# Performance work log

Hardware: AMD Instinct MI355X
Metric: run time of the kernel (lower is better)

The kernel has to match this reference:

```python
import jax, jax.numpy as jnp
import numpy as np

B, T, V, E, H, L = 128, 512, 32000, 1024, 1024, 2

def setup_inputs() -> dict:
    key = jax.random.key(0)
    ks = jax.random.split(key, 6)
    g = lambda k, shape: (jax.random.normal(k, shape, jnp.float32) * 0.02)
    return {
        "X": jax.random.randint(ks[0], (B, T), 0, V, dtype=jnp.int32),
        "emb": g(ks[1], (V, E)),
        "Wx0": g(ks[2], (E, 3 * H)),
        "Wh0": g(ks[3], (H, 3 * H)),
        "b0": jnp.zeros((2, 3 * H), jnp.float32),
        "Wx1": g(ks[4], (H, 3 * H)),
        "Wh1": g(ks[5], (H, 3 * H)),
        "b1": jnp.zeros((2, 3 * H), jnp.float32),
    }

def _gru_cell(x, h, Wx, Wh, b):
    # Keras GRUCell, reset_after=True, gate order (z, r, n)
    gx = x @ Wx + b[0]          # [B, 3H]
    gh = h @ Wh + b[1]          # [B, 3H]
    xz, xr, xn = jnp.split(gx, 3, axis=-1)
    hz, hr, hn = jnp.split(gh, 3, axis=-1)
    z = jax.nn.sigmoid(xz + hz)
    r = jax.nn.sigmoid(xr + hr)
    n = jnp.tanh(xn + r * hn)
    return z * h + (1.0 - z) * n

def reference(X, emb, Wx0, Wh0, b0, Wx1, Wh1, b1):
    Xe = emb[X]                         # [B, T, E] embedding lookup
    params = ((Wx0, Wh0, b0), (Wx1, Wh1, b1))
    h_init = tuple(jnp.zeros((X.shape[0], H), Xe.dtype) for _ in range(L))

    def step(carry, x_t):
        new_hs = []
        inp = x_t
        for h_prev, (Wx, Wh, b) in zip(carry, params):
            h_new = _gru_cell(inp, h_prev, Wx, Wh, b)
            new_hs.append(h_new)
            inp = h_new
        return tuple(new_hs), inp       # top-layer output per step

    final_state, outs = jax.lax.scan(step, h_init, jnp.swapaxes(Xe, 0, 1))
    output = jnp.swapaxes(outs, 0, 1)   # [B, T, H], return_sequences=True
    return (output,) + final_state      # (seq_output, h_layer0, h_layer1)
```

## Files before the change

kernel.cpp:

```cpp
#include <hip/hip_runtime.h>
#include <hip/hip_bf16.h>

#define B_ 128
#define T_ 512
#define E_ 1024
#define H_ 1024
#define V_ 32000

typedef __bf16 bf16_t;
typedef bf16_t bf16x8 __attribute__((ext_vector_type(8)));
typedef bf16_t bf16x4 __attribute__((ext_vector_type(4)));
typedef float  f32x4  __attribute__((ext_vector_type(4)));

__device__ __forceinline__ bf16x8 ld8(const bf16_t* p) {
  return *reinterpret_cast<const bf16x8*>(p);
}
__device__ __forceinline__ bf16x8 ld8f(const float* p) {
  f32x4 a = *reinterpret_cast<const f32x4*>(p);
  f32x4 b = *reinterpret_cast<const f32x4*>(p + 4);
  bf16x8 v;
  v[0] = (bf16_t)a[0]; v[1] = (bf16_t)a[1]; v[2] = (bf16_t)a[2]; v[3] = (bf16_t)a[3];
  v[4] = (bf16_t)b[0]; v[5] = (bf16_t)b[1]; v[6] = (bf16_t)b[2]; v[7] = (bf16_t)b[3];
  return v;
}

__global__ void detect_dtype(const unsigned short* __restrict__ p, int* flag) {
  __shared__ int s;
  if (threadIdx.x == 0) s = 0;
  __syncthreads();
  int cnt = 0;
  for (int i = threadIdx.x; i < 4096; i += blockDim.x) {
    const int e = (p[i] >> 7) & 0xFF;
    cnt += (e > 0x8F) ? 1 : 0;
  }
  atomicAdd(&s, cnt);
  __syncthreads();
  if (threadIdx.x == 0) *flag = (s > 8) ? 1 : 0;
}

__global__ void transpose_pack(const void* __restrict__ Wx,
                               const void* __restrict__ Wh,
                               bf16_t* __restrict__ WT,
                               const int* __restrict__ flag) {
  const int f32m = *flag;
  const int n  = blockIdx.x * 256 + threadIdx.x;
  const int k0 = blockIdx.y * 8;
  const void* src = (k0 < 1024) ? Wx : Wh;
  const int kb = (k0 < 1024) ? k0 : (k0 - 1024);
  bf16x8 v;
  if (f32m) {
    const float* s = (const float*)src;
#pragma unroll
    for (int j = 0; j < 8; ++j) v[j] = (bf16_t)s[(size_t)(kb + j) * 3072 + n];
  } else {
    const bf16_t* s = (const bf16_t*)src;
#pragma unroll
    for (int j = 0; j < 8; ++j) v[j] = s[(size_t)(kb + j) * 3072 + n];
  }
  *reinterpret_cast<bf16x8*>(WT + (size_t)n * 2048 + k0) = v;
}

__global__ void bias_pack(const void* __restrict__ b0, const void* __restrict__ b1,
                          float* __restrict__ biasf, const int* __restrict__ flag) {
  const int f32m = *flag;
  const int i = blockIdx.x * 256 + threadIdx.x;
  const void* src = (i < 6144) ? b0 : b1;
  const int j = (i < 6144) ? i : (i - 6144);
  biasf[i] = f32m ? ((const float*)src)[j] : (float)((const bf16_t*)src)[j];
}

__global__ void emb_pack(const void* __restrict__ emb, bf16_t* __restrict__ out,
                         const int* __restrict__ flag) {
  const int f32m = *flag;
  const size_t i = ((size_t)blockIdx.x * 256 + threadIdx.x) * 8;
  if (f32m) {
    const float* s = (const float*)emb + i;
    f32x4 a = *reinterpret_cast<const f32x4*>(s);
    f32x4 b = *reinterpret_cast<const f32x4*>(s + 4);
    bf16x8 v;
    v[0] = (bf16_t)a[0]; v[1] = (bf16_t)a[1]; v[2] = (bf16_t)a[2]; v[3] = (bf16_t)a[3];
    v[4] = (bf16_t)b[0]; v[5] = (bf16_t)b[1]; v[6] = (bf16_t)b[2]; v[7] = (bf16_t)b[3];
    *reinterpret_cast<bf16x8*>(out + i) = v;
  } else {
    *reinterpret_cast<bf16x8*>(out + i) = *reinterpret_cast<const bf16x8*>((const bf16_t*)emb + i);
  }
}

__device__ __forceinline__ unsigned ld_rlx(const unsigned* p) {
  return __hip_atomic_load(p, __ATOMIC_RELAXED, __HIP_MEMORY_SCOPE_AGENT);
}
__device__ __forceinline__ void wait_ge(const unsigned* p, unsigned tgt) {
  while (ld_rlx(p) < tgt) __builtin_amdgcn_s_sleep(1);
}
__device__ __forceinline__ void arrive(unsigned* cnt, unsigned* gen) {
  const unsigned old = __hip_atomic_fetch_add(cnt, 1u, __ATOMIC_RELAXED,
                                              __HIP_MEMORY_SCOPE_AGENT);
  if (old == 63u) {
    __hip_atomic_store(cnt, 0u, __ATOMIC_RELAXED, __HIP_MEMORY_SCOPE_AGENT);
    __hip_atomic_fetch_add(gen, 1u, __ATOMIC_RELEASE, __HIP_MEMORY_SCOPE_AGENT);
  }
}

__device__ __forceinline__ void gemm_half(const bf16_t* __restrict__ wz,
                                          const bf16_t* __restrict__ wr,
                                          const bf16_t* __restrict__ wn,
                                          const bf16_t* __restrict__ xr, int kq,
                                          f32x4& a0, f32x4& a1, f32x4& a2) {
#pragma unroll 4
  for (int kk = 0; kk < 32; ++kk) {
    const int k0 = kk * 32 + kq;
    const bf16x8 bfr = ld8(xr + k0);
    a0 = __builtin_amdgcn_mfma_f32_16x16x32_bf16(ld8(wz + k0), bfr, a0, 0, 0, 0);
    a1 = __builtin_amdgcn_mfma_f32_16x16x32_bf16(ld8(wr + k0), bfr, a1, 0, 0, 0);
    a2 = __builtin_amdgcn_mfma_f32_16x16x32_bf16(ld8(wn + k0), bfr, a2, 0, 0, 0);
  }
}
__device__ __forceinline__ void gemm_half_f32(const bf16_t* __restrict__ wz,
                                              const bf16_t* __restrict__ wr,
                                              const bf16_t* __restrict__ wn,
                                              const float* __restrict__ xr, int kq,
                                              f32x4& a0, f32x4& a1, f32x4& a2) {
#pragma unroll 4
  for (int kk = 0; kk < 32; ++kk) {
    const int k0 = kk * 32 + kq;
    const bf16x8 bfr = ld8f(xr + k0);
    a0 = __builtin_amdgcn_mfma_f32_16x16x32_bf16(ld8(wz + k0), bfr, a0, 0, 0, 0);
    a1 = __builtin_amdgcn_mfma_f32_16x16x32_bf16(ld8(wr + k0), bfr, a1, 0, 0, 0);
    a2 = __builtin_amdgcn_mfma_f32_16x16x32_bf16(ld8(wn + k0), bfr, a2, 0, 0, 0);
  }
}

__global__ void __launch_bounds__(256, 1)
gru_persistent(const int* __restrict__ X, const void* __restrict__ emb,
               const float* __restrict__ biasf,
               const bf16_t* __restrict__ W0T, const bf16_t* __restrict__ W1T,
               bf16_t* __restrict__ h0buf, bf16_t* __restrict__ h1buf,
               const bf16_t* __restrict__ embbf, void* __restrict__ outv,
               unsigned* __restrict__ sync, const int* __restrict__ flagp,
               int embws) {
  const int f32m = *flagp;

  const int blk   = blockIdx.x;
  const int xcd   = blk & 7;
  const int s     = blk >> 3;
  const int layer = xcd & 1;
  const int mblk  = s & 1;
  const int hblk  = (xcd >> 1) | ((s >> 1) << 2);

  const int tid  = threadIdx.x;
  const int wave = tid >> 6;
  const int lane = tid & 63;
  const int quad = lane >> 4;
  const int l15  = lane & 15;

  const int bb  = mblk * 64 + wave * 16 + l15;
  const int hc0 = hblk * 16;
  const int kq  = quad * 8;

  const bf16_t* WT = layer ? W1T : W0T;
  const bf16_t* wz = WT + (size_t)(hc0 + l15) * 2048;
  const bf16_t* wr = WT + (size_t)(1024 + hc0 + l15) * 2048;
  const bf16_t* wn = WT + (size_t)(2048 + hc0 + l15) * 2048;

  const float* bias = biasf + layer * 6144;
  const int hcq = hc0 + quad * 4;
  float bz[4], br[4], bxn[4], bhn[4];
#pragma unroll
  for (int r = 0; r < 4; ++r) {
    const int hc = hcq + r;
    bz[r]  = bias[hc]        + bias[3072 + hc];
    br[r]  = bias[1024 + hc] + bias[4096 + hc];
    bxn[r] = bias[2048 + hc];
    bhn[r] = bias[5120 + hc];
  }

  unsigned* ownCnt  = sync + (layer * 2 + mblk) * 64;
  unsigned* ownGen  = ownCnt + 32;
  unsigned* prodGen = sync + (0 * 2 + mblk) * 64 + 32;
  unsigned* consGen = sync + (1 * 2 + mblk) * 64 + 32;

  const int* Xrow = X + bb * T_;

  for (int t = 0; t < T_; ++t) {
    f32x4 az = {0,0,0,0}, ag = {0,0,0,0}, axn = {0,0,0,0}, ahn = {0,0,0,0};

    if (layer == 0) {
      int tok = Xrow[t];
      tok = (tok < 0) ? 0 : ((tok >= V_) ? (V_ - 1) : tok);
      if (embws) {
        gemm_half(wz, wr, wn, embbf + (size_t)tok * E_, kq, az, ag, axn);
      } else if (f32m) {
        gemm_half_f32(wz, wr, wn, (const float*)emb + (size_t)tok * E_, kq, az, ag, axn);
      } else {
        gemm_half(wz, wr, wn, (const bf16_t*)emb + (size_t)tok * E_, kq, az, ag, axn);
      }
    } else {
      if (tid == 0) { wait_ge(prodGen, (unsigned)(t + 1)); __threadfence(); }
      __syncthreads();
      gemm_half(wz, wr, wn,
                h0buf + (size_t)(t & 1) * (B_ * H_) + (size_t)bb * H_,
                kq, az, ag, axn);
    }

    float hp[4] = {0, 0, 0, 0};
    if (t > 0) {
      if (tid == 0) { wait_ge(ownGen, (unsigned)t); __threadfence(); }
      __syncthreads();
      const bf16_t* hrow = ((layer == 0) ? h0buf : h1buf) +
                           (size_t)((t - 1) & 1) * (B_ * H_) + (size_t)bb * H_;
      gemm_half(wz + 1024, wr + 1024, wn + 1024, hrow, kq, az, ag, ahn);
      const bf16x4 hv = *reinterpret_cast<const bf16x4*>(hrow + hcq);
#pragma unroll
      for (int r = 0; r < 4; ++r) hp[r] = (float)hv[r];
    }

    float hf[4];
    bf16x4 hnew;
#pragma unroll
    for (int r = 0; r < 4; ++r) {
      const float z  = 1.f / (1.f + __expf(-(az[r] + bz[r])));
      const float rg = 1.f / (1.f + __expf(-(ag[r] + br[r])));
      const float a  = (axn[r] + bxn[r]) + rg * (ahn[r] + bhn[r]);
      const float e  = __expf(-2.f * fabsf(a));
      const float tn = (1.f - e) / (1.f + e);
      const float n  = (a >= 0.f) ? tn : -tn;
      hf[r] = z * hp[r] + (1.f - z) * n;
      hnew[r] = (bf16_t)hf[r];
    }

    if (layer == 0 && t >= 2) {
      if (tid == 0) wait_ge(consGen, (unsigned)(t - 1));
      __syncthreads();
    }

    bf16_t* hwb = ((layer == 0) ? h0buf : h1buf) +
                  (size_t)(t & 1) * (B_ * H_) + (size_t)bb * H_ + hcq;
    *reinterpret_cast<bf16x4*>(hwb) = hnew;

    if (layer == 1) {
      const size_t oi = ((size_t)bb * T_ + t) * H_ + hcq;
      if (f32m) *reinterpret_cast<f32x4*>((float*)outv + oi) = f32x4{hf[0], hf[1], hf[2], hf[3]};
      else      *reinterpret_cast<bf16x4*>((bf16_t*)outv + oi) = hnew;
    }
    if (t == T_ - 1) {
      const size_t oi = (size_t)B_ * T_ * H_ + (size_t)layer * (B_ * H_) +
                        (size_t)bb * H_ + hcq;
      if (f32m) *reinterpret_cast<f32x4*>((float*)outv + oi) = f32x4{hf[0], hf[1], hf[2], hf[3]};
      else      *reinterpret_cast<bf16x4*>((bf16_t*)outv + oi) = hnew;
    }

    __syncthreads();
    if (tid == 0) { __threadfence(); arrive(ownCnt, ownGen); }
  }
}

extern "C" void kernel_launch(void* const* d_in, const int* in_sizes, int n_in,
                              void* d_out, int out_size, void* d_ws, size_t ws_size,
                              hipStream_t stream) {
  const int*  X   = (const int*)d_in[0];
  const void* emb = d_in[1];
  const void* Wx0 = d_in[2];
  const void* Wh0 = d_in[3];
  const void* b0  = d_in[4];
  const void* Wx1 = d_in[5];
  const void* Wh1 = d_in[6];
  const void* b1  = d_in[7];

  char*     ws    = (char*)d_ws;
  bf16_t*   W0T   = (bf16_t*)(ws);
  bf16_t*   W1T   = (bf16_t*)(ws + 12582912);
  bf16_t*   h0buf = (bf16_t*)(ws + 25165824);
  bf16_t*   h1buf = (bf16_t*)(ws + 25690112);
  float*    biasf = (float*) (ws + 26214400);
  int*      flag  = (int*)   (ws + 26263552);
  unsigned* syncp = (unsigned*)(ws + 26263680);
  bf16_t*   embbf = (bf16_t*)(ws + 26267648);
  int embws = (ws_size >= 91803648ull) ? 1 : 0;

  hipMemsetAsync(syncp, 0, 1024, stream);
  detect_dtype<<<1, 256, 0, stream>>>((const unsigned short*)emb, flag);
  transpose_pack<<<dim3(12, 256), 256, 0, stream>>>(Wx0, Wh0, W0T, flag);
  transpose_pack<<<dim3(12, 256), 256, 0, stream>>>(Wx1, Wh1, W1T, flag);
  bias_pack<<<48, 256, 0, stream>>>(b0, b1, biasf, flag);
  if (embws) emb_pack<<<16000, 256, 0, stream>>>(emb, embbf, flag);

  void* args[] = {(void*)&X, (void*)&emb, (void*)&biasf, (void*)&W0T, (void*)&W1T,
                  (void*)&h0buf, (void*)&h1buf, (void*)&embbf, (void*)&d_out,
                  (void*)&syncp, (void*)&flag, (void*)&embws};
  hipLaunchCooperativeKernel((void*)gru_persistent, dim3(256), dim3(256),
                             args, 0, stream);
}
```

Measured before the change: 22.26 ms.

## Add producer waves that prefetch next-step input rows into LDS via async loads

Doubles the block to 512 threads. Four extra producer waves use global_load_lds to fill a swizzled 128KB LDS buffer with the next timestep's input rows (embedding rows for layer 0, h0 rows for layer 1) while the compute waves run the recurrent GEMM. The input-projection GEMM then reads its B operand from LDS, taking that global load off the critical path. Output stores move after the arrive signal and the unroll factor rises to 8. The cost is more LDS, more threads per block, and an extra barrier phase, and layer 1 now waits on the producer one step ahead.

```diff
diff --git a/kernel.cpp b/kernel.cpp
--- a/kernel.cpp
+++ b/kernel.cpp
@@ -22,6 +22,12 @@
   v[0] = (bf16_t)a[0]; v[1] = (bf16_t)a[1]; v[2] = (bf16_t)a[2]; v[3] = (bf16_t)a[3];
   v[4] = (bf16_t)b[0]; v[5] = (bf16_t)b[1]; v[6] = (bf16_t)b[2]; v[7] = (bf16_t)b[3];
   return v;
+}
+
+__device__ __forceinline__ void gl_lds16(const void* g, void* l) {
+  typedef const unsigned int __attribute__((address_space(1)))* gp_t;
+  typedef unsigned int __attribute__((address_space(3)))* lp_t;
+  __builtin_amdgcn_global_load_lds((gp_t)g, (lp_t)l, 16, 0, 0);
 }
 
 __global__ void detect_dtype(const unsigned short* __restrict__ p, int* flag) {
@@ -106,7 +112,7 @@
                                           const bf16_t* __restrict__ wn,
                                           const bf16_t* __restrict__ xr, int kq,
                                           f32x4& a0, f32x4& a1, f32x4& a2) {
-#pragma unroll 4
+#pragma unroll 8
   for (int kk = 0; kk < 32; ++kk) {
     const int k0 = kk * 32 + kq;
     const bf16x8 bfr = ld8(xr + k0);
@@ -130,7 +136,7 @@
   }
 }
 
-__global__ void __launch_bounds__(256, 1)
+__global__ void __launch_bounds__(512, 1)
 gru_persistent(const int* __restrict__ X, const void* __restrict__ emb,
                const float* __restrict__ biasf,
                const bf16_t* __restrict__ W0T, const bf16_t* __restrict__ W1T,
@@ -138,7 +144,11 @@
                const bf16_t* __restrict__ embbf, void* __restrict__ outv,
                unsigned* __restrict__ sync, const int* __restrict__ flagp,
                int embws) {
+  __shared__ char ldsX[131072] __attribute__((aligned(128)));
+
   const int f32m = *flagp;
+  const int use_lds_x = (embws || !f32m) ? 1 : 0;
+  const bf16_t* embsrc = embws ? embbf : (const bf16_t*)emb;
 
   const int blk   = blockIdx.x;
   const int xcd   = blk & 7;
@@ -153,7 +163,9 @@
   const int quad = lane >> 4;
   const int l15  = lane & 15;
 
-  const int bb  = mblk * 64 + wave * 16 + l15;
+  const int cw  = wave & 3;
+  const int r   = cw * 16 + l15;
+  const int bb  = mblk * 64 + r;
   const int hc0 = hblk * 16;
   const int kq  = quad * 8;
 
@@ -166,12 +178,12 @@
   const int hcq = hc0 + quad * 4;
   float bz[4], br[4], bxn[4], bhn[4];
 #pragma unroll
-  for (int r = 0; r < 4; ++r) {
-    const int hc = hcq + r;
-    bz[r]  = bias[hc]        + bias[3072 + hc];
-    br[r]  = bias[1024 + hc] + bias[4096 + hc];
-    bxn[r] = bias[2048 + hc];
-    bhn[r] = bias[5120 + hc];
+  for (int q = 0; q < 4; ++q) {
+    const int hc = hcq + q;
+    bz[q]  = bias[hc]        + bias[3072 + hc];
+    br[q]  = bias[1024 + hc] + bias[4096 + hc];
+    bxn[q] = bias[2048 + hc];
+    bhn[q] = bias[5120 + hc];
   }
 
   unsigned* ownCnt  = sync + (layer * 2 + mblk) * 64;
@@ -181,76 +193,136 @@
 
   const int* Xrow = X + bb * T_;
 
+  auto fill_x = [&](int tt) {
+    const int pw = wave - 4;
+    int mytok = 0;
+    if (layer == 0) {
+      const int rr = pw * 16 + (lane & 15);
+      int tk = X[(mblk * 64 + rr) * T_ + tt];
+      mytok = (tk < 0) ? 0 : ((tk >= V_) ? (V_ - 1) : tk);
+    }
+    const unsigned lco = (unsigned)(lane * 16);
+#pragma unroll
+    for (int jj = 0; jj < 32; ++jj) {
+      const int row  = pw * 16 + (jj >> 1);
+      const int half = jj & 1;
+      const char* rowp;
+      if (layer == 0) {
+        const int tok = __shfl(mytok, jj >> 1, 64);
+        rowp = (const char*)(embsrc + (size_t)tok * E_);
+      } else {
+        rowp = (const char*)(h0buf + (size_t)(tt & 1) * (B_ * H_) +
+                             (size_t)(mblk * 64 + row) * H_);
+      }
+      const unsigned c = lco ^ ((unsigned)(row & 7) << 4);
+      gl_lds16(rowp + half * 1024 + c, &ldsX[(size_t)(pw * 32 + jj) * 1024]);
+    }
+  };
+
+  if (wave >= 4 && use_lds_x) {
+    if (layer == 1) {
+      if (lane == 0) wait_ge(prodGen, 1u);
+      __threadfence();
+    }
+    fill_x(0);
+  }
+  __syncthreads();
+
+  const unsigned rx = ((unsigned)(r & 7)) << 4;
+  const char* lxp = &ldsX[(size_t)r * 2048];
+
   for (int t = 0; t < T_; ++t) {
     f32x4 az = {0,0,0,0}, ag = {0,0,0,0}, axn = {0,0,0,0}, ahn = {0,0,0,0};
-
-    if (layer == 0) {
-      int tok = Xrow[t];
-      tok = (tok < 0) ? 0 : ((tok >= V_) ? (V_ - 1) : tok);
-      if (embws) {
-        gemm_half(wz, wr, wn, embbf + (size_t)tok * E_, kq, az, ag, axn);
-      } else if (f32m) {
-        gemm_half_f32(wz, wr, wn, (const float*)emb + (size_t)tok * E_, kq, az, ag, axn);
-      } else {
-        gemm_half(wz, wr, wn, (const bf16_t*)emb + (size_t)tok * E_, kq, az, ag, axn);
-      }
-    } else {
-      if (tid == 0) { wait_ge(prodGen, (unsigned)(t + 1)); __threadfence(); }
-      __syncthreads();
-      gemm_half(wz, wr, wn,
-                h0buf + (size_t)(t & 1) * (B_ * H_) + (size_t)bb * H_,
-                kq, az, ag, axn);
-    }
-
     float hp[4] = {0, 0, 0, 0};
-    if (t > 0) {
-      if (tid == 0) { wait_ge(ownGen, (unsigned)t); __threadfence(); }
-      __syncthreads();
-      const bf16_t* hrow = ((layer == 0) ? h0buf : h1buf) +
-                           (size_t)((t - 1) & 1) * (B_ * H_) + (size_t)bb * H_;
-      gemm_half(wz + 1024, wr + 1024, wn + 1024, hrow, kq, az, ag, ahn);
-      const bf16x4 hv = *reinterpret_cast<const bf16x4*>(hrow + hcq);
-#pragma unroll
-      for (int r = 0; r < 4; ++r) hp[r] = (float)hv[r];
-    }
-
     float hf[4];
     bf16x4 hnew;
-#pragma unroll
-    for (int r = 0; r < 4; ++r) {
-      const float z  = 1.f / (1.f + __expf(-(az[r] + bz[r])));
-      const float rg = 1.f / (1.f + __expf(-(ag[r] + br[r])));
-      const float a  = (axn[r] + bxn[r]) + rg * (ahn[r] + bhn[r]);
-      const float e  = __expf(-2.f * fabsf(a));
-      const float tn = (1.f - e) / (1.f + e);
-      const float n  = (a >= 0.f) ? tn : -tn;
-      hf[r] = z * hp[r] + (1.f - z) * n;
-      hnew[r] = (bf16_t)hf[r];
-    }
-
-    if (layer == 0 && t >= 2) {
-      if (tid == 0) wait_ge(consGen, (unsigned)(t - 1));
+
+    if (!use_lds_x) {
+      if (tid == 0 && layer == 1) { wait_ge(prodGen, (unsigned)(t + 1)); __threadfence(); }
       __syncthreads();
     }
 
-    bf16_t* hwb = ((layer == 0) ? h0buf : h1buf) +
-                  (size_t)(t & 1) * (B_ * H_) + (size_t)bb * H_ + hcq;
-    *reinterpret_cast<bf16x4*>(hwb) = hnew;
-
-    if (layer == 1) {
-      const size_t oi = ((size_t)bb * T_ + t) * H_ + hcq;
-      if (f32m) *reinterpret_cast<f32x4*>((float*)outv + oi) = f32x4{hf[0], hf[1], hf[2], hf[3]};
-      else      *reinterpret_cast<bf16x4*>((bf16_t*)outv + oi) = hnew;
-    }
-    if (t == T_ - 1) {
-      const size_t oi = (size_t)B_ * T_ * H_ + (size_t)layer * (B_ * H_) +
-                        (size_t)bb * H_ + hcq;
-      if (f32m) *reinterpret_cast<f32x4*>((float*)outv + oi) = f32x4{hf[0], hf[1], hf[2], hf[3]};
-      else      *reinterpret_cast<bf16x4*>((bf16_t*)outv + oi) = hnew;
-    }
-
+    if (wave < 4) {
+      if (use_lds_x) {
+#pragma unroll 8
+        for (int kk = 0; kk < 32; ++kk) {
+          const int k0 = kk * 32 + kq;
+          const bf16x8 bfr =
+              *reinterpret_cast<const bf16x8*>(lxp + (((unsigned)(2 * k0)) ^ rx));
+          az  = __builtin_amdgcn_mfma_f32_16x16x32_bf16(ld8(wz + k0), bfr, az, 0, 0, 0);
+          ag  = __builtin_amdgcn_mfma_f32_16x16x32_bf16(ld8(wr + k0), bfr, ag, 0, 0, 0);
+          axn = __builtin_amdgcn_mfma_f32_16x16x32_bf16(ld8(wn + k0), bfr, axn, 0, 0, 0);
+        }
+      } else {
+        if (layer == 0) {
+          int tok = Xrow[t];
+          tok = (tok < 0) ? 0 : ((tok >= V_) ? (V_ - 1) : tok);
+          gemm_half_f32(wz, wr, wn, (const float*)emb + (size_t)tok * E_, kq, az, ag, axn);
+        } else {
+          gemm_half(wz, wr, wn,
+                    h0buf + (size_t)(t & 1) * (B_ * H_) + (size_t)bb * H_,
+                    kq, az, ag, axn);
+        }
+      }
+    }
+
+    if (tid == 0 && t > 0) { wait_ge(ownGen, (unsigned)t); __threadfence(); }
     __syncthreads();
+
+    if (wave < 4) {
+      if (t > 0) {
+        const bf16_t* hrow = ((layer == 0) ? h0buf : h1buf) +
+                             (size_t)((t - 1) & 1) * (B_ * H_) + (size_t)bb * H_;
+        const bf16x4 hv = *reinterpret_cast<const bf16x4*>(hrow + hcq);
+        gemm_half(wz + 1024, wr + 1024, wn + 1024, hrow, kq, az, ag, ahn);
+#pragma unroll
+        for (int q = 0; q < 4; ++q) hp[q] = (float)hv[q];
+      }
+
+#pragma unroll
+      for (int q = 0; q < 4; ++q) {
+        const float z  = 1.f / (1.f + __expf(-(az[q] + bz[q])));
+        const float rg = 1.f / (1.f + __expf(-(ag[q] + br[q])));
+        const float a  = (axn[q] + bxn[q]) + rg * (ahn[q] + bhn[q]);
+        const float e  = __expf(-2.f * fabsf(a));
+        const float tn = (1.f - e) / (1.f + e);
+        const float n  = (a >= 0.f) ? tn : -tn;
+        hf[q] = z * hp[q] + (1.f - z) * n;
+        hnew[q] = (bf16_t)hf[q];
+      }
+
+      if (layer == 0 && t >= 2) {
+        if (lane == 0) wait_ge(consGen, (unsigned)(t - 1));
+      }
+      bf16_t* hwb = ((layer == 0) ? h0buf : h1buf) +
+                    (size_t)(t & 1) * (B_ * H_) + (size_t)bb * H_ + hcq;
+      *reinterpret_cast<bf16x4*>(hwb) = hnew;
+    } else {
+      if (use_lds_x && t + 1 < T_) {
+        if (layer == 1) {
+          if (lane == 0) wait_ge(prodGen, (unsigned)(t + 2));
+          __threadfence();
+        }
+        fill_x(t + 1);
+      }
+    }
+    __syncthreads();
+
     if (tid == 0) { __threadfence(); arrive(ownCnt, ownGen); }
+
+    if (wave < 4) {
+      if (layer == 1) {
+        const size_t oi = ((size_t)bb * T_ + t) * H_ + hcq;
+        if (f32m) *reinterpret_cast<f32x4*>((float*)outv + oi) = f32x4{hf[0], hf[1], hf[2], hf[3]};
+        else      *reinterpret_cast<bf16x4*>((bf16_t*)outv + oi) = hnew;
+      }
+      if (t == T_ - 1) {
+        const size_t oi = (size_t)B_ * T_ * H_ + (size_t)layer * (B_ * H_) +
+                          (size_t)bb * H_ + hcq;
+        if (f32m) *reinterpret_cast<f32x4*>((float*)outv + oi) = f32x4{hf[0], hf[1], hf[2], hf[3]};
+        else      *reinterpret_cast<bf16x4*>((bf16_t*)outv + oi) = hnew;
+      }
+    }
   }
 }
 
@@ -287,6 +359,6 @@
   void* args[] = {(void*)&X, (void*)&emb, (void*)&biasf, (void*)&W0T, (void*)&W1T,
                   (void*)&h0buf, (void*)&h1buf, (void*)&embbf, (void*)&d_out,
                   (void*)&syncp, (void*)&flag, (void*)&embws};
-  hipLaunchCooperativeKernel((void*)gru_persistent, dim3(256), dim3(256),
+  hipLaunchCooperativeKernel((void*)gru_persistent, dim3(256), dim3(512),
                              args, 0, stream);
 }
```

After: 27.71 ms. +24.5%, slower.
